# Kernel optimization log

Hardware: AMD Instinct MI355X
Metric: run time of the kernel (lower is better)

The kernel has to match this reference:

```python
import jax, jax.numpy as jnp
import numpy as np

B, NR_BOX, D = 512, 18, 2048
NR_OBJ = NR_BOX - 2
K = 3
NUM_CLASSES = 174
NUM_CAT = 321


def setup_inputs() -> dict:
    key = jax.random.key(0)
    k1, k2, k3, k4, k5, k6 = jax.random.split(key, 6)
    obj_fea = jax.random.normal(k1, (B, NR_BOX, D), dtype=jnp.float32)
    # cooccurrence: nonnegative, sparse-ish, first (pad) column zero as in the torch code
    cooc = jax.random.uniform(k2, (NUM_CLASSES, NUM_CAT), dtype=jnp.float32)
    mask = jax.random.uniform(k3, (NUM_CLASSES, NUM_CAT)) < 0.5
    cooc = jnp.where(mask, cooc, 0.0).at[:, 0].set(0.0)
    obj_indicator = jax.random.randint(k4, (B, NR_BOX), 0, 2).astype(jnp.int32)
    obj_category = jax.random.randint(k5, (B, NR_BOX), 0, NUM_CAT).astype(jnp.int32)
    labels = jax.random.randint(k6, (B,), 0, NUM_CLASSES).astype(jnp.int32)
    return {
        'obj_fea': obj_fea,
        'cooccurrence': cooc,
        'obj_indicator': obj_indicator,
        'obj_category': obj_category,
        'labels': labels,
    }


def reference(obj_fea, cooccurrence, obj_indicator, obj_category, labels):
    Bn, nr_box, d = obj_fea.shape
    nr_obj = nr_box - 2
    ind = obj_indicator[:, 2:]          # (B, nr_obj)
    cats = obj_category[:, 2:]          # (B, nr_obj)
    ori_comp = obj_fea.mean(axis=1)     # (B, d)
    objs = obj_fea[:, 2:]               # (B, nr_obj, d), hands dropped
    label_onehot = jax.nn.one_hot(labels, NUM_CLASSES, dtype=obj_fea.dtype)  # (B, C)

    # W[i, b, j] = cooccurrence[labels[i], cats[b, j]]  (candidate weights per sample i)
    cooc_lab = cooccurrence[labels]                 # (B, NUM_CAT)
    W = cooc_lab[:, cats]                           # (B, B, nr_obj)
    eye = jnp.eye(Bn, dtype=bool)
    W = jnp.where(eye[:, :, None], 0.0, W)          # exclude own video (cand_obj[i] = 0)
    Wf = W.reshape(Bn, Bn * nr_obj)

    # softmax(log w) over nonzero support == w / sum(w); sample via categorical on log-weights
    logits = jnp.where(Wf > 0, jnp.log(jnp.where(Wf > 0, Wf, 1.0)), -jnp.inf)
    has_cand = (Wf > 0).any(axis=1) & (ind != 0).any(axis=1)  # (B,)

    rng = jax.random.key(42)
    r1, r2, r3 = jax.random.split(rng, 3)
    sel = jax.random.categorical(r1, logits, shape=(K, Bn)).T   # (B, K) flat candidate ids
    batch_idx = sel // nr_obj
    box_idx = sel % nr_obj
    sel_fea = objs[batch_idx, box_idx]              # (B, K, d)
    sel_label = label_onehot[batch_idx]             # (B, K, C)

    lam = jax.random.uniform(r2, (Bn, 1, 1), dtype=obj_fea.dtype)  # Beta(1,1)==U(0,1), one per sample
    slots = jax.random.randint(r3, (Bn, K), 0, nr_obj)
    own_fea = jnp.take_along_axis(objs, slots[:, :, None], axis=1)  # (B, K, d)

    mixed_fea = own_fea * lam + sel_fea * (1.0 - lam)
    mixed_label = label_onehot[:, None, :] * lam + sel_label * (1.0 - lam)

    # fallback path: mean of own objects + own one-hot label, repeated K times
    fb_fea = jnp.broadcast_to(objs.mean(axis=1)[:, None, :], mixed_fea.shape)
    fb_label = jnp.broadcast_to(label_onehot[:, None, :], mixed_label.shape)
    m = has_cand[:, None, None]
    mix_fea = jnp.where(m, mixed_fea, fb_fea)
    mix_label = jnp.where(m, mixed_label, fb_label)
    return ori_comp, mix_fea, mix_label
```

## Files before the change

kernel.cpp:

```cpp
#include <hip/hip_runtime.h>
#include <stdint.h>
#include <math.h>

#define NBOX 18
#define BB 512
#define DD 2048
#define NOBJ 16
#define KK 3
#define NCLS 174
#define NCAT 321
#define NQ 4
#define QCAND 2048
#define NPART 16

__host__ __device__ __forceinline__ uint32_t rotl32(uint32_t x, int d) {
  return (x << d) | (x >> (32 - d));
}

__host__ __device__ __forceinline__ void threefry2x32(uint32_t k0, uint32_t k1,
                                                      uint32_t x0, uint32_t x1,
                                                      uint32_t& o0, uint32_t& o1) {
  uint32_t ks2 = k0 ^ k1 ^ 0x1BD11BDAu;
  x0 += k0; x1 += k1;
#define TFR(r) x0 += x1; x1 = rotl32(x1, r); x1 ^= x0;
#define R4A TFR(13) TFR(15) TFR(26) TFR(6)
#define R4B TFR(17) TFR(29) TFR(16) TFR(24)
  R4A x0 += k1;  x1 += ks2 + 1u;
  R4B x0 += ks2; x1 += k0 + 2u;
  R4A x0 += k0;  x1 += k1 + 3u;
  R4B x0 += k1;  x1 += ks2 + 4u;
  R4A x0 += ks2; x1 += k0 + 5u;
#undef R4A
#undef R4B
#undef TFR
  o0 = x0; o1 = x1;
}

__device__ __forceinline__ float bits_to_unit(uint32_t bits) {
  float f = __uint_as_float((bits >> 9) | 0x3f800000u);
  return f - 1.0f;
}

__device__ __forceinline__ void gload_lds16(const void* g, void* l) {
  __builtin_amdgcn_global_load_lds(
      (const __attribute__((address_space(1))) unsigned int*)g,
      (__attribute__((address_space(3))) unsigned int*)l, 16, 0, 0);
}

__global__ __launch_bounds__(256) void sample_stream_kernel(
    const float* __restrict__ obj_fea, const float* __restrict__ cooc,
    const int* __restrict__ obj_cat, const int* __restrict__ labels,
    uint32_t r1h, uint32_t r1l,
    unsigned long long* __restrict__ part, int* __restrict__ cnts,
    float* __restrict__ ori, float4* __restrict__ m16ws) {
  const int gb = blockIdx.x;
  const int b = gb >> 2;
  const int q = gb & 3;
  const int tid = threadIdx.x;
  const int lane = tid & 63;
  const int wid = tid >> 6;

  __shared__ float4 slds[NBOX * 128];
  __shared__ unsigned short jl[QCAND];
  __shared__ float wl[QCAND];

  const int col0 = q << 7;
  const float4* fea4 = (const float4*)obj_fea;
  const float4* gbase = fea4 + (size_t)b * NBOX * 512 + col0;
#pragma unroll
  for (int i = 0; i < 9; ++i) {
    const int L = wid * 9 + i;
    const int r = L >> 1, hh = L & 1;
    const float4* g = gbase + (size_t)r * 512 + hh * 64 + lane;
    gload_lds16((const void*)g, (void*)((char*)slds + (size_t)L * 1024));
  }
  __builtin_amdgcn_sched_barrier(0);

  const int lab = labels[b];
  const float* crow = cooc + (size_t)lab * NCAT;
  const int seg = wid << 9;
  const int jbase = (q << 11) + seg;
  int cnt = 0;
#pragma unroll 1
  for (int c = 0; c < 8; ++c) {
    int j = jbase + (c << 6) + lane;
    int jb = j >> 4;
    float w = 0.0f;
    if (jb != b) w = crow[obj_cat[jb * NBOX + 2 + (j & 15)]];
    unsigned long long m = __ballot(w > 0.0f);
    if (w > 0.0f) {
      int rank = __popcll(m & ((1ull << lane) - 1ull));
      jl[seg + cnt + rank] = (unsigned short)j;
      wl[seg + cnt + rank] = w;
    }
    cnt += __popcll(m);
  }

  const uint32_t cbase0 = ((uint32_t)b) << 13;
  const uint32_t kstep = 1u << 22;
  float bw0 = 0.f, bt0 = 1.f, bw1 = 0.f, bt1 = 1.f, bw2 = 0.f, bt2 = 1.f;
  int bj0 = 0, bj1 = 0, bj2 = 0;
#pragma unroll 1
  for (int p = lane; p < cnt; p += 64) {
    uint32_t j = jl[seg + p];
    float w = wl[seg + p];
    uint32_t cc = cbase0 + j;
    uint32_t x0, x1, y0, y1, z0, z1;
    threefry2x32(r1h, r1l, 0u, cc, x0, x1);
    threefry2x32(r1h, r1l, 0u, cc + kstep, y0, y1);
    threefry2x32(r1h, r1l, 0u, cc + 2u * kstep, z0, z1);
    float t0 = -__log2f(fmaxf(bits_to_unit(x0 ^ x1), 1.1920929e-07f));
    float t1 = -__log2f(fmaxf(bits_to_unit(y0 ^ y1), 1.1920929e-07f));
    float t2 = -__log2f(fmaxf(bits_to_unit(z0 ^ z1), 1.1920929e-07f));
    if (w * bt0 > bw0 * t0) { bw0 = w; bt0 = t0; bj0 = (int)j; }
    if (w * bt1 > bw1 * t1) { bw1 = w; bt1 = t1; bj1 = (int)j; }
    if (w * bt2 > bw2 * t2) { bw2 = w; bt2 = t2; bj2 = (int)j; }
  }
#pragma unroll
  for (int mm = 1; mm < 64; mm <<= 1) {
    float ow, ot; int oj;
    ow = __shfl_xor(bw0, mm, 64); ot = __shfl_xor(bt0, mm, 64); oj = __shfl_xor(bj0, mm, 64);
    { float lv = ow * bt0, rv = bw0 * ot;
      if (lv > rv || (lv == rv && oj < bj0)) { bw0 = ow; bt0 = ot; bj0 = oj; } }
    ow = __shfl_xor(bw1, mm, 64); ot = __shfl_xor(bt1, mm, 64); oj = __shfl_xor(bj1, mm, 64);
    { float lv = ow * bt1, rv = bw1 * ot;
      if (lv > rv || (lv == rv && oj < bj1)) { bw1 = ow; bt1 = ot; bj1 = oj; } }
    ow = __shfl_xor(bw2, mm, 64); ot = __shfl_xor(bt2, mm, 64); oj = __shfl_xor(bj2, mm, 64);
    { float lv = ow * bt2, rv = bw2 * ot;
      if (lv > rv || (lv == rv && oj < bj2)) { bw2 = ow; bt2 = ot; bj2 = oj; } }
  }
  if (lane == 0) {
    const int pw = (q << 2) + wid;
    const size_t pb = (size_t)b * KK * NPART;
    part[pb + 0 * NPART + pw] =
        ((unsigned long long)__float_as_uint(bw0 / bt0) << 32) | (uint32_t)(8192 - bj0);
    part[pb + 1 * NPART + pw] =
        ((unsigned long long)__float_as_uint(bw1 / bt1) << 32) | (uint32_t)(8192 - bj1);
    part[pb + 2 * NPART + pw] =
        ((unsigned long long)__float_as_uint(bw2 / bt2) << 32) | (uint32_t)(8192 - bj2);
    cnts[b * NPART + pw] = cnt;
  }

  __syncthreads();
  const int rh = tid & 1;
  const int col = tid >> 1;
  float4 acc = make_float4(0.f, 0.f, 0.f, 0.f);
#pragma unroll
  for (int r = 0; r < 9; ++r) {
    float4 t = slds[(rh * 9 + r) * 128 + col];
    acc.x += t.x; acc.y += t.y; acc.z += t.z; acc.w += t.w;
  }
  float4 oth;
  oth.x = __shfl_xor(acc.x, 1, 64); oth.y = __shfl_xor(acc.y, 1, 64);
  oth.z = __shfl_xor(acc.z, 1, 64); oth.w = __shfl_xor(acc.w, 1, 64);
  if (rh == 0) {
    float4 S = make_float4(acc.x + oth.x, acc.y + oth.y, acc.z + oth.z, acc.w + oth.w);
    float4 v0 = slds[col];
    float4 v1 = slds[128 + col];
    const float i18 = 1.0f / 18.0f, i16 = 1.0f / 16.0f;
    const size_t oidx = (size_t)b * 512 + col0 + col;
    ((float4*)ori)[oidx] = make_float4(S.x * i18, S.y * i18, S.z * i18, S.w * i18);
    m16ws[oidx] = make_float4((S.x - v0.x - v1.x) * i16, (S.y - v0.y - v1.y) * i16,
                              (S.z - v0.z - v1.z) * i16, (S.w - v0.w - v1.w) * i16);
  }
}

__global__ __launch_bounds__(256) void mix_kernel(
    const float* __restrict__ obj_fea, const int* __restrict__ obj_ind,
    const int* __restrict__ labels,
    const unsigned long long* __restrict__ part, const int* __restrict__ cnts,
    const float4* __restrict__ m16ws,
    uint32_t r2h, uint32_t r2l, uint32_t r3bh, uint32_t r3bl,
    float* __restrict__ mixf, float* __restrict__ mixl) {
  const int bx = blockIdx.x;
  const int b = bx >> 1;
  const int h = bx & 1;
  const int tid = threadIdx.x;
  const int off = (h << 8) + tid;

  __shared__ int s_sel[KK];
  __shared__ int s_slots[KK];
  __shared__ float s_lam;
  __shared__ int s_cnt;
  __shared__ int s_any;

  if (tid < NPART) {
    unsigned long long p0 = part[((size_t)b * KK + 0) * NPART + tid];
    unsigned long long p1 = part[((size_t)b * KK + 1) * NPART + tid];
    unsigned long long p2 = part[((size_t)b * KK + 2) * NPART + tid];
    int ct = cnts[b * NPART + tid];
#pragma unroll
    for (int mm = 1; mm < NPART; mm <<= 1) {
      unsigned long long qq;
      qq = __shfl_xor(p0, mm, 64); if (qq > p0) p0 = qq;
      qq = __shfl_xor(p1, mm, 64); if (qq > p1) p1 = qq;
      qq = __shfl_xor(p2, mm, 64); if (qq > p2) p2 = qq;
      ct |= __shfl_xor(ct, mm, 64);
    }
    if (tid == 0) {
      s_sel[0] = 8192 - (int)(p0 & 0xFFFFFFFFull);
      s_sel[1] = 8192 - (int)(p1 & 0xFFFFFFFFull);
      s_sel[2] = 8192 - (int)(p2 & 0xFFFFFFFFull);
      s_cnt = ct;
    }
  } else if (tid < NPART + KK) {
    const int k = tid - NPART;
    uint32_t s0, s1;
    threefry2x32(r3bh, r3bl, 0u, (uint32_t)(b * KK + k), s0, s1);
    s_slots[k] = (int)((s0 ^ s1) & 15u);
  } else if (tid == NPART + KK) {
    uint32_t c0, c1;
    threefry2x32(r2h, r2l, 0u, (uint32_t)b, c0, c1);
    s_lam = bits_to_unit(c0 ^ c1);
  } else if (tid == NPART + KK + 1) {
    int any = 0;
#pragma unroll
    for (int oo = 0; oo < NOBJ; ++oo) any |= (obj_ind[b * NBOX + 2 + oo] != 0);
    s_any = any;
  }
  __syncthreads();

  const int hc = (s_cnt != 0) && s_any;
  const float l = s_lam, l1 = 1.0f - l;
  const float4* fea4 = (const float4*)obj_fea;
  float4* mixf4 = (float4*)mixf;
  if (hc) {
#pragma unroll 1
    for (int k = 0; k < KK; ++k) {
      int s = s_sel[k];
      int bi = s >> 4, bo = s & 15, sl = s_slots[k];
      float4 a = fea4[((size_t)b * NBOX + 2 + sl) * 512 + off];
      float4 e = fea4[((size_t)bi * NBOX + 2 + bo) * 512 + off];
      float4 ov;
      ov.x = a.x * l + e.x * l1; ov.y = a.y * l + e.y * l1;
      ov.z = a.z * l + e.z * l1; ov.w = a.w * l + e.w * l1;
      mixf4[((size_t)b * KK + k) * 512 + off] = ov;
    }
  } else {
    float4 m16 = m16ws[(size_t)b * 512 + off];
#pragma unroll
    for (int k = 0; k < KK; ++k) mixf4[((size_t)b * KK + k) * 512 + off] = m16;
  }

  if (h == 0 && tid < NCLS) {
    int lb = labels[b];
#pragma unroll 1
    for (int k = 0; k < KK; ++k) {
      float val;
      if (hc) {
        int ls = labels[s_sel[k] >> 4];
        val = (tid == lb ? l : 0.0f) + (tid == ls ? l1 : 0.0f);
      } else {
        val = (tid == lb) ? 1.0f : 0.0f;
      }
      mixl[(size_t)(b * KK + k) * NCLS + tid] = val;
    }
  }
}

extern "C" void kernel_launch(void* const* d_in, const int* in_sizes, int n_in,
                              void* d_out, int out_size, void* d_ws, size_t ws_size,
                              hipStream_t stream) {
  (void)in_sizes; (void)n_in; (void)out_size; (void)ws_size;
  const float* obj_fea = (const float*)d_in[0];
  const float* cooc    = (const float*)d_in[1];
  const int* obj_ind   = (const int*)d_in[2];
  const int* obj_cat   = (const int*)d_in[3];
  const int* labels    = (const int*)d_in[4];

  float* out  = (float*)d_out;
  float* ori  = out;
  float* mixf = out + (size_t)BB * DD;
  float* mixl = mixf + (size_t)BB * KK * DD;

  char* ws = (char*)d_ws;
  unsigned long long* part = (unsigned long long*)ws;
  int* cnts = (int*)(ws + (size_t)BB * KK * NPART * 8);
  float4* m16ws = (float4*)(ws + 1024 * 1024);

  uint32_t r1h, r1l, r2h, r2l, r3h, r3l;
  threefry2x32(0u, 42u, 0u, 0u, r1h, r1l);
  threefry2x32(0u, 42u, 0u, 1u, r2h, r2l);
  threefry2x32(0u, 42u, 0u, 2u, r3h, r3l);
  uint32_t r3bh, r3bl;
  threefry2x32(r3h, r3l, 0u, 1u, r3bh, r3bl);

  hipLaunchKernelGGL(sample_stream_kernel, dim3(BB * NQ), dim3(256), 0, stream,
                     obj_fea, cooc, obj_cat, labels, r1h, r1l,
                     part, cnts, ori, m16ws);
  hipLaunchKernelGGL(mix_kernel, dim3(BB * 2), dim3(256), 0, stream,
                     obj_fea, obj_ind, labels, part, cnts, m16ws,
                     r2h, r2l, r3bh, r3bl, mixf, mixl);
}
```

Baseline: 48.49 us.

## Split candidate race across eight blocks per sample and drop fallback-mean workspace

The sampling kernel now uses eight blocks per sample, each covering 1024 candidates, where before it used four blocks of 2048. The per-sample mean is computed only by the first two blocks, with direct register loads instead of global-to-LDS async copies. The fallback mean of the 16 objects is no longer written to a workspace; the mix kernel recomputes it from the features only for samples without candidates. This aims to raise parallelism and shorten the serial candidate loop. In exchange, the mix kernel must merge twice as many partial results, and blocks do uneven work.

```diff
diff --git a/kernel.cpp b/kernel.cpp
--- a/kernel.cpp
+++ b/kernel.cpp
@@ -9,9 +9,9 @@
 #define KK 3
 #define NCLS 174
 #define NCAT 321
-#define NQ 4
-#define QCAND 2048
-#define NPART 16
+#define NE 8
+#define ECAND 1024
+#define NPART 32
 
 __host__ __device__ __forceinline__ uint32_t rotl32(uint32_t x, int d) {
   return (x << d) | (x >> (32 - d));
@@ -41,48 +41,46 @@
   return f - 1.0f;
 }
 
-__device__ __forceinline__ void gload_lds16(const void* g, void* l) {
-  __builtin_amdgcn_global_load_lds(
-      (const __attribute__((address_space(1))) unsigned int*)g,
-      (__attribute__((address_space(3))) unsigned int*)l, 16, 0, 0);
-}
-
-__global__ __launch_bounds__(256) void sample_stream_kernel(
+__global__ __launch_bounds__(256) void race_stream_kernel(
     const float* __restrict__ obj_fea, const float* __restrict__ cooc,
     const int* __restrict__ obj_cat, const int* __restrict__ labels,
     uint32_t r1h, uint32_t r1l,
     unsigned long long* __restrict__ part, int* __restrict__ cnts,
-    float* __restrict__ ori, float4* __restrict__ m16ws) {
+    float* __restrict__ ori) {
   const int gb = blockIdx.x;
-  const int b = gb >> 2;
-  const int q = gb & 3;
+  const int b = gb >> 3;
+  const int e = gb & 7;
   const int tid = threadIdx.x;
   const int lane = tid & 63;
   const int wid = tid >> 6;
 
-  __shared__ float4 slds[NBOX * 128];
-  __shared__ unsigned short jl[QCAND];
-  __shared__ float wl[QCAND];
-
-  const int col0 = q << 7;
-  const float4* fea4 = (const float4*)obj_fea;
-  const float4* gbase = fea4 + (size_t)b * NBOX * 512 + col0;
-#pragma unroll
-  for (int i = 0; i < 9; ++i) {
-    const int L = wid * 9 + i;
-    const int r = L >> 1, hh = L & 1;
-    const float4* g = gbase + (size_t)r * 512 + hh * 64 + lane;
-    gload_lds16((const void*)g, (void*)((char*)slds + (size_t)L * 1024));
-  }
-  __builtin_amdgcn_sched_barrier(0);
+  __shared__ unsigned short jl[ECAND];
+  __shared__ float wl[ECAND];
+
+  if (e < 2) {
+    const float4* src = (const float4*)obj_fea + (size_t)b * NBOX * 512 + (e << 8) + tid;
+    float4 a[9];
+#pragma unroll
+    for (int r = 0; r < 9; ++r) a[r] = src[(size_t)r * 512];
+    float4 S = a[0];
+#pragma unroll
+    for (int r = 1; r < 9; ++r) { S.x += a[r].x; S.y += a[r].y; S.z += a[r].z; S.w += a[r].w; }
+#pragma unroll
+    for (int r = 0; r < 9; ++r) a[r] = src[(size_t)(9 + r) * 512];
+#pragma unroll
+    for (int r = 0; r < 9; ++r) { S.x += a[r].x; S.y += a[r].y; S.z += a[r].z; S.w += a[r].w; }
+    const float i18 = 1.0f / 18.0f;
+    ((float4*)ori)[(size_t)b * 512 + (e << 8) + tid] =
+        make_float4(S.x * i18, S.y * i18, S.z * i18, S.w * i18);
+  }
 
   const int lab = labels[b];
   const float* crow = cooc + (size_t)lab * NCAT;
-  const int seg = wid << 9;
-  const int jbase = (q << 11) + seg;
+  const int seg = wid << 8;
+  const int jbase = (e << 10) + seg;
   int cnt = 0;
 #pragma unroll 1
-  for (int c = 0; c < 8; ++c) {
+  for (int c = 0; c < 4; ++c) {
     int j = jbase + (c << 6) + lane;
     int jb = j >> 4;
     float w = 0.0f;
@@ -130,7 +128,7 @@
       if (lv > rv || (lv == rv && oj < bj2)) { bw2 = ow; bt2 = ot; bj2 = oj; } }
   }
   if (lane == 0) {
-    const int pw = (q << 2) + wid;
+    const int pw = (e << 2) + wid;
     const size_t pb = (size_t)b * KK * NPART;
     part[pb + 0 * NPART + pw] =
         ((unsigned long long)__float_as_uint(bw0 / bt0) << 32) | (uint32_t)(8192 - bj0);
@@ -140,36 +138,12 @@
         ((unsigned long long)__float_as_uint(bw2 / bt2) << 32) | (uint32_t)(8192 - bj2);
     cnts[b * NPART + pw] = cnt;
   }
-
-  __syncthreads();
-  const int rh = tid & 1;
-  const int col = tid >> 1;
-  float4 acc = make_float4(0.f, 0.f, 0.f, 0.f);
-#pragma unroll
-  for (int r = 0; r < 9; ++r) {
-    float4 t = slds[(rh * 9 + r) * 128 + col];
-    acc.x += t.x; acc.y += t.y; acc.z += t.z; acc.w += t.w;
-  }
-  float4 oth;
-  oth.x = __shfl_xor(acc.x, 1, 64); oth.y = __shfl_xor(acc.y, 1, 64);
-  oth.z = __shfl_xor(acc.z, 1, 64); oth.w = __shfl_xor(acc.w, 1, 64);
-  if (rh == 0) {
-    float4 S = make_float4(acc.x + oth.x, acc.y + oth.y, acc.z + oth.z, acc.w + oth.w);
-    float4 v0 = slds[col];
-    float4 v1 = slds[128 + col];
-    const float i18 = 1.0f / 18.0f, i16 = 1.0f / 16.0f;
-    const size_t oidx = (size_t)b * 512 + col0 + col;
-    ((float4*)ori)[oidx] = make_float4(S.x * i18, S.y * i18, S.z * i18, S.w * i18);
-    m16ws[oidx] = make_float4((S.x - v0.x - v1.x) * i16, (S.y - v0.y - v1.y) * i16,
-                              (S.z - v0.z - v1.z) * i16, (S.w - v0.w - v1.w) * i16);
-  }
 }
 
 __global__ __launch_bounds__(256) void mix_kernel(
     const float* __restrict__ obj_fea, const int* __restrict__ obj_ind,
     const int* __restrict__ labels,
     const unsigned long long* __restrict__ part, const int* __restrict__ cnts,
-    const float4* __restrict__ m16ws,
     uint32_t r2h, uint32_t r2l, uint32_t r3bh, uint32_t r3bl,
     float* __restrict__ mixf, float* __restrict__ mixl) {
   const int bx = blockIdx.x;
@@ -230,16 +204,24 @@
       int s = s_sel[k];
       int bi = s >> 4, bo = s & 15, sl = s_slots[k];
       float4 a = fea4[((size_t)b * NBOX + 2 + sl) * 512 + off];
-      float4 e = fea4[((size_t)bi * NBOX + 2 + bo) * 512 + off];
+      float4 ee = fea4[((size_t)bi * NBOX + 2 + bo) * 512 + off];
       float4 ov;
-      ov.x = a.x * l + e.x * l1; ov.y = a.y * l + e.y * l1;
-      ov.z = a.z * l + e.z * l1; ov.w = a.w * l + e.w * l1;
+      ov.x = a.x * l + ee.x * l1; ov.y = a.y * l + ee.y * l1;
+      ov.z = a.z * l + ee.z * l1; ov.w = a.w * l + ee.w * l1;
       mixf4[((size_t)b * KK + k) * 512 + off] = ov;
     }
   } else {
-    float4 m16 = m16ws[(size_t)b * 512 + off];
-#pragma unroll
-    for (int k = 0; k < KK; ++k) mixf4[((size_t)b * KK + k) * 512 + off] = m16;
+    const float4* src = fea4 + (size_t)b * NBOX * 512 + off;
+    float4 S = make_float4(0.f, 0.f, 0.f, 0.f);
+#pragma unroll
+    for (int r = 2; r < NBOX; ++r) {
+      float4 t = src[(size_t)r * 512];
+      S.x += t.x; S.y += t.y; S.z += t.z; S.w += t.w;
+    }
+    const float i16 = 1.0f / 16.0f;
+    float4 ov = make_float4(S.x * i16, S.y * i16, S.z * i16, S.w * i16);
+#pragma unroll
+    for (int k = 0; k < KK; ++k) mixf4[((size_t)b * KK + k) * 512 + off] = ov;
   }
 
   if (h == 0 && tid < NCLS) {
@@ -276,7 +258,6 @@
   char* ws = (char*)d_ws;
   unsigned long long* part = (unsigned long long*)ws;
   int* cnts = (int*)(ws + (size_t)BB * KK * NPART * 8);
-  float4* m16ws = (float4*)(ws + 1024 * 1024);
 
   uint32_t r1h, r1l, r2h, r2l, r3h, r3l;
   threefry2x32(0u, 42u, 0u, 0u, r1h, r1l);
@@ -285,10 +266,10 @@
   uint32_t r3bh, r3bl;
   threefry2x32(r3h, r3l, 0u, 1u, r3bh, r3bl);
 
-  hipLaunchKernelGGL(sample_stream_kernel, dim3(BB * NQ), dim3(256), 0, stream,
+  hipLaunchKernelGGL(race_stream_kernel, dim3(BB * NE), dim3(256), 0, stream,
                      obj_fea, cooc, obj_cat, labels, r1h, r1l,
-                     part, cnts, ori, m16ws);
+                     part, cnts, ori);
   hipLaunchKernelGGL(mix_kernel, dim3(BB * 2), dim3(256), 0, stream,
-                     obj_fea, obj_ind, labels, part, cnts, m16ws,
+                     obj_fea, obj_ind, labels, part, cnts,
                      r2h, r2l, r3bh, r3bl, mixf, mixl);
 }
```

Result: slower. 55.74 us (+14.9%).
